# Optimization experiments

Measured on AMD Instinct MI355X. Metric: run time of the kernel, lower is better.

Reference implementation:

```python
import jax, jax.numpy as jnp
import numpy as np

N_NODES = 50000
N_EDGES = 800000
IN_DIM = 128
HIDDEN = 64
HEADS = 4
N_GRAPHS = 256
NEG_SLOPE = 0.2  # PyG GATConv default


def gat_conv(x, src, dst, W, a_src, a_dst, b):
    """PyG-style GATConv (concat=True), eval mode (no dropout).
    x: [N, F_in]; src/dst: [E] (self-loops already included);
    W: [H*C, F_in]; a_src/a_dst: [H, C]; b: [H*C].
    """
    N = x.shape[0]
    H, C = a_src.shape
    h = (x @ W.T).reshape(N, H, C)                      # [N, H, C]
    alo = (h * a_src[None]).sum(-1)                     # [N, H]
    ahi = (h * a_dst[None]).sum(-1)                     # [N, H]
    e = jax.nn.leaky_relu(alo[src] + ahi[dst], NEG_SLOPE)  # [E, H]
    # segment softmax over destination neighborhoods
    m = jax.ops.segment_max(e, dst, num_segments=N)     # [N, H]
    ex = jnp.exp(e - m[dst])
    denom = jax.ops.segment_sum(ex, dst, num_segments=N)
    alpha = ex / (denom[dst] + 1e-16)                   # [E, H]
    out = jax.ops.segment_sum(h[src] * alpha[:, :, None], dst, num_segments=N)
    return out.reshape(N, H * C) + b


def setup_inputs() -> dict:
    key = jax.random.key(0)
    ks = jax.random.split(key, 24)
    p = lambda k, s: (jax.random.normal(k, s, jnp.float32) * 0.1)
    x = jax.random.normal(ks[0], (N_NODES, IN_DIM), jnp.float32)
    edge_index = jax.random.randint(ks[1], (2, N_EDGES), 0, N_NODES, jnp.int64 if jax.config.jax_enable_x64 else jnp.int32)
    batch_idx = jnp.sort(jax.random.randint(ks[2], (N_NODES,), 0, N_GRAPHS))
    HC = HIDDEN * HEADS
    return {
        "x": x, "edge_index": edge_index, "batch_idx": batch_idx,
        "W1": p(ks[3], (HC, IN_DIM)), "as1": p(ks[4], (HEADS, HIDDEN)), "ad1": p(ks[5], (HEADS, HIDDEN)), "b1": jnp.zeros((HC,), jnp.float32),
        "W2": p(ks[6], (HC, HC)), "as2": p(ks[7], (HEADS, HIDDEN)), "ad2": p(ks[8], (HEADS, HIDDEN)), "b2": jnp.zeros((HC,), jnp.float32),
        "W3": p(ks[9], (HIDDEN, HC)), "as3": p(ks[10], (1, HIDDEN)), "ad3": p(ks[11], (1, HIDDEN)), "b3": jnp.zeros((HIDDEN,), jnp.float32),
        "Wc1": p(ks[12], (HIDDEN, HIDDEN)), "bc1": jnp.zeros((HIDDEN,), jnp.float32),
        "Wc2": p(ks[13], (1, HIDDEN)), "bc2": jnp.zeros((1,), jnp.float32),
        "Wr1": p(ks[14], (HIDDEN, HIDDEN)), "br1": jnp.zeros((HIDDEN,), jnp.float32),
        "Wr2": p(ks[15], (1, HIDDEN)), "br2": jnp.zeros((1,), jnp.float32),
    }


def reference(x, edge_index, batch_idx, W1, as1, ad1, b1, W2, as2, ad2, b2, W3, as3, ad3, b3, Wc1, bc1, Wc2, bc2, Wr1, br1, Wr2, br2):
    N = x.shape[0]
    loops = jnp.arange(N, dtype=edge_index.dtype)
    src = jnp.concatenate([edge_index[0], loops])  # add_self_loops=True (PyG default)
    dst = jnp.concatenate([edge_index[1], loops])
    h = jax.nn.elu(gat_conv(x, src, dst, W1, as1, ad1, b1))
    h = jax.nn.elu(gat_conv(h, src, dst, W2, as2, ad2, b2))
    h = jax.nn.elu(gat_conv(h, src, dst, W3, as3, ad3, b3))  # [N, HIDDEN]
    # global mean pool over graphs
    cnt = jax.ops.segment_sum(jnp.ones((N,), h.dtype), batch_idx, num_segments=N_GRAPHS)
    g = jax.ops.segment_sum(h, batch_idx, num_segments=N_GRAPHS) / jnp.maximum(cnt, 1.0)[:, None]
    cls_logit = (jax.nn.relu(g @ Wc1.T + bc1) @ Wc2.T + bc2).reshape(-1)
    reg_pred = (jax.nn.relu(g @ Wr1.T + br1) @ Wr2.T + br2).reshape(-1)
    return (cls_logit, reg_pred)
```

## Files before the change

### kernel.cpp

```cpp
#include <hip/hip_runtime.h>

#define N_NODES 50000
#define N_EDGES 800000
#define EP_EDGES (N_EDGES + N_NODES)
#define N_GRAPHS 256
#define NBLK_SCAN ((N_NODES + 255) / 256)
#define POOL_CHUNK ((N_NODES + 255) / 256)

typedef unsigned short u16;
typedef __attribute__((ext_vector_type(8))) short s8v;
typedef __attribute__((ext_vector_type(4))) float f4v;

__device__ __forceinline__ u16 fb(float f) {
  unsigned u = __float_as_uint(f);
  return (u16)((u + 0x7fffu + ((u >> 16) & 1u)) >> 16);
}
__device__ __forceinline__ float bfl(unsigned p) {
  return __uint_as_float(p << 16);
}
__device__ __forceinline__ float bfh(unsigned p) {
  return __uint_as_float(p & 0xffff0000u);
}
__device__ __forceinline__ float bff(u16 s) {
  return __uint_as_float(((unsigned)s) << 16);
}

#define F2B_N0 (N_NODES * 128)
#define F2B_N1 (F2B_N0 + 32768)
#define F2B_N2 (F2B_N1 + 65536)
#define F2B_N3 (F2B_N2 + 16384)
__global__ void f2b4(const float* __restrict__ x, const float* __restrict__ w1,
                     const float* __restrict__ w2, const float* __restrict__ w3,
                     u16* __restrict__ xb, u16* __restrict__ w1b,
                     u16* __restrict__ w2b, u16* __restrict__ w3b) {
  int i = blockIdx.x * 256 + threadIdx.x;
  if (i < F2B_N0) xb[i] = fb(x[i]);
  else if (i < F2B_N1) w1b[i - F2B_N0] = fb(w1[i - F2B_N0]);
  else if (i < F2B_N2) w2b[i - F2B_N1] = fb(w2[i - F2B_N1]);
  else if (i < F2B_N3) w3b[i - F2B_N2] = fb(w3[i - F2B_N2]);
}

__global__ __launch_bounds__(256) void gemm128(
    const u16* __restrict__ A, const u16* __restrict__ W,
    u16* __restrict__ C, int M, int Nout, int K) {
  __shared__ u16 As[128][40];
  __shared__ u16 Bs[128][40];
  const int t = threadIdx.x;
  const int m0 = blockIdx.y * 128, n0 = blockIdx.x * 128;
  const int rq = t >> 2, q = t & 3;
  const int w = t >> 6, lane = t & 63;
  const int wi = (w & 1) * 64, wj = (w >> 1) * 64;
  const int quad = lane >> 4, fr = lane & 15;

  f4v acc[4][4] = {};
  for (int k0 = 0; k0 < K; k0 += 32) {
    uint4 av[2], bv[2];
#pragma unroll
    for (int g = 0; g < 2; ++g) {
      int r = rq + g * 64;
      int m = m0 + r;
      av[g] = (m < M) ? *(const uint4*)&A[(size_t)m * K + k0 + q * 8]
                      : make_uint4(0, 0, 0, 0);
      bv[g] = *(const uint4*)&W[(size_t)(n0 + r) * K + k0 + q * 8];
    }
    __syncthreads();
#pragma unroll
    for (int g = 0; g < 2; ++g) {
      *(uint4*)&As[rq + g * 64][q * 8] = av[g];
      *(uint4*)&Bs[rq + g * 64][q * 8] = bv[g];
    }
    __syncthreads();
    s8v af[4], bf_[4];
#pragma unroll
    for (int i = 0; i < 4; ++i) {
      af[i] = *(const s8v*)&As[wi + i * 16 + fr][quad * 8];
      bf_[i] = *(const s8v*)&Bs[wj + i * 16 + fr][quad * 8];
    }
#pragma unroll
    for (int i = 0; i < 4; ++i)
#pragma unroll
      for (int j = 0; j < 4; ++j)
        acc[i][j] =
            __builtin_amdgcn_mfma_f32_16x16x32_bf16(af[i], bf_[j], acc[i][j], 0, 0, 0);
  }
#pragma unroll
  for (int i = 0; i < 4; ++i) {
    int rbase = m0 + wi + i * 16 + quad * 4;
#pragma unroll
    for (int j = 0; j < 4; ++j) {
      int col = n0 + wj + j * 16 + fr;
#pragma unroll
      for (int r = 0; r < 4; ++r) {
        int row = rbase + r;
        if (row < M) C[(size_t)row * Nout + col] = fb(acc[i][j][r]);
      }
    }
  }
}

__global__ __launch_bounds__(256) void gemm_bf16(
    const u16* __restrict__ A, const u16* __restrict__ W,
    u16* __restrict__ C, int M, int Nout, int K) {
  __shared__ u16 As[64][40];
  __shared__ u16 Bs[64][40];
  const int t = threadIdx.x;
  const int m0 = blockIdx.y * 64, n0 = blockIdx.x * 64;
  const int r = t >> 2, c = t & 3;
  const int w = t >> 6, lane = t & 63;
  const int mi = (w & 1) * 32, ni = (w >> 1) * 32;
  const int quad = lane >> 4, fr = lane & 15;

  f4v c00{}, c01{}, c10{}, c11{};
  for (int k0 = 0; k0 < K; k0 += 32) {
    uint4 av = make_uint4(0, 0, 0, 0);
    int m = m0 + r;
    if (m < M) av = *(const uint4*)&A[(size_t)m * K + k0 + c * 8];
    uint4 bv = *(const uint4*)&W[(size_t)(n0 + r) * K + k0 + c * 8];
    __syncthreads();
    *(uint4*)&As[r][c * 8] = av;
    *(uint4*)&Bs[r][c * 8] = bv;
    __syncthreads();
    s8v a0 = *(const s8v*)&As[mi + fr][quad * 8];
    s8v a1 = *(const s8v*)&As[mi + 16 + fr][quad * 8];
    s8v b0 = *(const s8v*)&Bs[ni + fr][quad * 8];
    s8v b1 = *(const s8v*)&Bs[ni + 16 + fr][quad * 8];
    c00 = __builtin_amdgcn_mfma_f32_16x16x32_bf16(a0, b0, c00, 0, 0, 0);
    c01 = __builtin_amdgcn_mfma_f32_16x16x32_bf16(a0, b1, c01, 0, 0, 0);
    c10 = __builtin_amdgcn_mfma_f32_16x16x32_bf16(a1, b0, c10, 0, 0, 0);
    c11 = __builtin_amdgcn_mfma_f32_16x16x32_bf16(a1, b1, c11, 0, 0, 0);
  }
  const int col = n0 + ni + fr;
#pragma unroll
  for (int i = 0; i < 4; ++i) {
    int row = m0 + mi + quad * 4 + i;
    if (row < M) {
      C[(size_t)row * Nout + col] = fb(c00[i]);
      C[(size_t)row * Nout + col + 16] = fb(c01[i]);
    }
    int row2 = row + 16;
    if (row2 < M) {
      C[(size_t)row2 * Nout + col] = fb(c10[i]);
      C[(size_t)row2 * Nout + col + 16] = fb(c11[i]);
    }
  }
}

__global__ void k_hist(const int* __restrict__ ei, int* __restrict__ deg) {
  int e = blockIdx.x * 256 + threadIdx.x;
  if (e >= EP_EDGES) return;
  int d = (e < N_EDGES) ? ei[N_EDGES + e] : e - N_EDGES;
  atomicAdd(&deg[d], 1);
}

__global__ void k_scan_local(const int* __restrict__ deg,
                             int* __restrict__ rowstart,
                             int* __restrict__ bsum) {
  __shared__ int sh[256];
  const int tid = threadIdx.x;
  const int i = blockIdx.x * 256 + tid;
  int v = (i < N_NODES) ? deg[i] : 0;
  sh[tid] = v;
  __syncthreads();
  for (int off = 1; off < 256; off <<= 1) {
    int add = (tid >= off) ? sh[tid - off] : 0;
    __syncthreads();
    sh[tid] += add;
    __syncthreads();
  }
  if (i < N_NODES) rowstart[i] = sh[tid] - v;
  if (tid == 255) bsum[blockIdx.x] = sh[255];
}

__global__ void k_scan_bsum(int* __restrict__ bsum, int* __restrict__ boff) {
  __shared__ int sh[256];
  const int tid = threadIdx.x;
  int v = (tid < NBLK_SCAN) ? bsum[tid] : 0;
  sh[tid] = v;
  __syncthreads();
  for (int off = 1; off < 256; off <<= 1) {
    int add = (tid >= off) ? sh[tid - off] : 0;
    __syncthreads();
    sh[tid] += add;
    __syncthreads();
  }
  boff[tid] = sh[tid] - v;
}

__global__ void k_scan_add(int* __restrict__ rowstart,
                           const int* __restrict__ boff) {
  int i = blockIdx.x * 256 + threadIdx.x;
  if (i < N_NODES) rowstart[i] += boff[i >> 8];
  if (i == N_NODES) rowstart[N_NODES] = EP_EDGES;
}

__global__ void k_scatter(const int* __restrict__ ei,
                          const int* __restrict__ rowstart,
                          int* __restrict__ fill, int* __restrict__ esrc) {
  int e = blockIdx.x * 256 + threadIdx.x;
  if (e >= EP_EDGES) return;
  int s, d;
  if (e < N_EDGES) { s = ei[e]; d = ei[N_EDGES + e]; }
  else             { s = d = e - N_EDGES; }
  int pos = rowstart[d] + atomicAdd(&fill[d], 1);
  esrc[pos] = s;
}

__global__ __launch_bounds__(256) void attn_scores4(
    const u16* __restrict__ h, const float* __restrict__ a_src,
    const float* __restrict__ a_dst, float* __restrict__ alo,
    float* __restrict__ ahi) {
  const int t = threadIdx.x;
  const int n = blockIdx.x * 4 + (t >> 6);
  const int lane = t & 63;
  const int head = lane >> 4, l16 = lane & 15;
  const int ch = head * 64 + l16 * 4;
  uint2 hv = *(const uint2*)&h[(size_t)n * 256 + ch];
  float4 asv = *(const float4*)&a_src[ch];
  float4 adv = *(const float4*)&a_dst[ch];
  float v0 = bfl(hv.x), v1 = bfh(hv.x), v2 = bfl(hv.y), v3 = bfh(hv.y);
  float s = v0 * asv.x + v1 * asv.y + v2 * asv.z + v3 * asv.w;
  float d = v0 * adv.x + v1 * adv.y + v2 * adv.z + v3 * adv.w;
#pragma unroll
  for (int off = 8; off; off >>= 1) {
    s += __shfl_xor(s, off, 64);
    d += __shfl_xor(d, off, 64);
  }
  if (l16 == 0) {
    alo[n * 4 + head] = s;
    ahi[n * 4 + head] = d;
  }
}

__global__ __launch_bounds__(256) void attn_scores1(
    const u16* __restrict__ h, const float* __restrict__ a_src,
    const float* __restrict__ a_dst, float* __restrict__ alo,
    float* __restrict__ ahi) {
  const int t = threadIdx.x;
  const int n = blockIdx.x * 4 + (t >> 6);
  const int lane = t & 63;
  float v = bff(h[(size_t)n * 64 + lane]);
  float s = v * a_src[lane];
  float d = v * a_dst[lane];
#pragma unroll
  for (int off = 32; off; off >>= 1) {
    s += __shfl_xor(s, off, 64);
    d += __shfl_xor(d, off, 64);
  }
  if (lane == 0) {
    alo[n] = s;
    ahi[n] = d;
  }
}

__global__ __launch_bounds__(64) void agg3_4(
    const int* __restrict__ rowstart, const int* __restrict__ esrc,
    const u16* __restrict__ hbuf, const float* __restrict__ alo,
    const float* __restrict__ ahi, const float* __restrict__ bias,
    u16* __restrict__ feat) {
  const int d = blockIdx.x;
  const int lane = threadIdx.x;
  const int head = lane >> 4;
  const int l16 = lane & 15;
  const int c = lane * 4;
  const int s0 = rowstart[d], s1 = rowstart[d + 1];
  const float ah = ahi[d * 4 + head];

  float sm = 0.f;
  for (int j = s0 + l16; j < s1; j += 16) {
    int s = esrc[j];
    float e = alo[s * 4 + head] + ah;
    e = e > 0.f ? e : 0.2f * e;
    sm += __expf(e);
  }
#pragma unroll
  for (int off = 8; off; off >>= 1) sm += __shfl_xor(sm, off, 64);
  const float linv = 1.f / (sm + 1e-16f);

  float o0 = 0.f, o1 = 0.f, o2 = 0.f, o3 = 0.f;
  for (int j = s0; j < s1; j += 4) {
    int ss[4];
    float wq[4];
#pragma unroll
    for (int q = 0; q < 4; ++q) {
      int jj = j + q;
      int sv = esrc[jj < EP_EDGES ? jj : EP_EDGES - 1];
      ss[q] = (jj < s1) ? sv : d;
    }
#pragma unroll
    for (int q = 0; q < 4; ++q) {
      float e = alo[ss[q] * 4 + head] + ah;
      e = e > 0.f ? e : 0.2f * e;
      wq[q] = (j + q < s1) ? __expf(e) * linv : 0.f;
    }
    uint2 hv[4];
#pragma unroll
    for (int q = 0; q < 4; ++q)
      hv[q] = *(const uint2*)&hbuf[(size_t)ss[q] * 256 + c];
#pragma unroll
    for (int q = 0; q < 4; ++q) {
      o0 += wq[q] * bfl(hv[q].x);
      o1 += wq[q] * bfh(hv[q].x);
      o2 += wq[q] * bfl(hv[q].y);
      o3 += wq[q] * bfh(hv[q].y);
    }
  }
  float4 bv = *(const float4*)&bias[c];
  float v0 = o0 + bv.x, v1 = o1 + bv.y, v2 = o2 + bv.z, v3 = o3 + bv.w;
  v0 = v0 > 0.f ? v0 : __expf(v0) - 1.f;
  v1 = v1 > 0.f ? v1 : __expf(v1) - 1.f;
  v2 = v2 > 0.f ? v2 : __expf(v2) - 1.f;
  v3 = v3 > 0.f ? v3 : __expf(v3) - 1.f;
  uint2 pv;
  pv.x = (unsigned)fb(v0) | ((unsigned)fb(v1) << 16);
  pv.y = (unsigned)fb(v2) | ((unsigned)fb(v3) << 16);
  *(uint2*)&feat[(size_t)d * 256 + c] = pv;
}

__global__ __launch_bounds__(64) void agg3_1(
    const int* __restrict__ rowstart, const int* __restrict__ esrc,
    const u16* __restrict__ hbuf, const float* __restrict__ alo,
    const float* __restrict__ ahi, const float* __restrict__ bias,
    float* __restrict__ feat) {
  const int d = blockIdx.x;
  const int t = threadIdx.x;
  const int s0 = rowstart[d], s1 = rowstart[d + 1];
  const float ah = ahi[d];

  float sm = 0.f;
  for (int j = s0 + t; j < s1; j += 64) {
    int s = esrc[j];
    float e = alo[s] + ah;
    e = e > 0.f ? e : 0.2f * e;
    sm += __expf(e);
  }
#pragma unroll
  for (int off = 32; off; off >>= 1) sm += __shfl_xor(sm, off, 64);
  const float linv = 1.f / (sm + 1e-16f);

  float o = 0.f;
  for (int j = s0; j < s1; j += 4) {
    int ss[4];
    float wq[4];
#pragma unroll
    for (int q = 0; q < 4; ++q) {
      int jj = j + q;
      int sv = esrc[jj < EP_EDGES ? jj : EP_EDGES - 1];
      ss[q] = (jj < s1) ? sv : d;
    }
#pragma unroll
    for (int q = 0; q < 4; ++q) {
      float e = alo[ss[q]] + ah;
      e = e > 0.f ? e : 0.2f * e;
      wq[q] = (j + q < s1) ? __expf(e) * linv : 0.f;
    }
    u16 hv[4];
#pragma unroll
    for (int q = 0; q < 4; ++q) hv[q] = hbuf[(size_t)ss[q] * 64 + t];
#pragma unroll
    for (int q = 0; q < 4; ++q) o += wq[q] * bff(hv[q]);
  }
  float v = o + bias[t];
  feat[(size_t)d * 64 + t] = v > 0.f ? v : __expf(v) - 1.f;
}

__global__ __launch_bounds__(64) void pool_seg(
    const float* __restrict__ feat, const int* __restrict__ batch,
    float* __restrict__ gsum, float* __restrict__ gcnt) {
  const int b = blockIdx.x;
  const int t = threadIdx.x;
  int n0 = b * POOL_CHUNK;
  int n1 = n0 + POOL_CHUNK;
  if (n1 > N_NODES) n1 = N_NODES;
  if (n0 >= n1) return;
  int g = batch[n0];
  float acc = 0.f;
  int cnt = 0;
  for (int n = n0; n < n1; ++n) {
    int gn = batch[n];
    if (gn != g) {
      atomicAdd(&gsum[g * 64 + t], acc);
      if (t == 0) atomicAdd(&gcnt[g], (float)cnt);
      acc = 0.f; cnt = 0; g = gn;
    }
    acc += feat[(size_t)n * 64 + t];
    ++cnt;
  }
  atomicAdd(&gsum[g * 64 + t], acc);
  if (t == 0) atomicAdd(&gcnt[g], (float)cnt);
}

__global__ void heads(const float* __restrict__ gsum,
                      const float* __restrict__ gcnt,
                      const float* __restrict__ Wc1, const float* __restrict__ bc1,
                      const float* __restrict__ Wc2, const float* __restrict__ bc2,
                      const float* __restrict__ Wr1, const float* __restrict__ br1,
                      const float* __restrict__ Wr2, const float* __restrict__ br2,
                      float* __restrict__ out) {
  __shared__ float g[64];
  const int gi = blockIdx.x, j = threadIdx.x;
  float cnt = gcnt[gi];
  cnt = cnt < 1.f ? 1.f : cnt;
  g[j] = gsum[gi * 64 + j] / cnt;
  __syncthreads();
  float hc = bc1[j], hr = br1[j];
#pragma unroll 8
  for (int c = 0; c < 64; ++c) {
    float gv = g[c];
    hc += gv * Wc1[j * 64 + c];
    hr += gv * Wr1[j * 64 + c];
  }
  hc = fmaxf(hc, 0.f) * Wc2[j];
  hr = fmaxf(hr, 0.f) * Wr2[j];
#pragma unroll
  for (int off = 32; off; off >>= 1) {
    hc += __shfl_down(hc, off, 64);
    hr += __shfl_down(hr, off, 64);
  }
  if (j == 0) {
    out[gi] = hc + bc2[0];
    out[N_GRAPHS + gi] = hr + br2[0];
  }
}

extern "C" void kernel_launch(void* const* d_in, const int* in_sizes, int n_in,
                              void* d_out, int out_size, void* d_ws,
                              size_t ws_size, hipStream_t stream) {
  const float* x   = (const float*)d_in[0];
  const int* ei    = (const int*)d_in[1];
  const int* batch = (const int*)d_in[2];
  const float* W1  = (const float*)d_in[3];
  const float* as1 = (const float*)d_in[4];
  const float* ad1 = (const float*)d_in[5];
  const float* b1  = (const float*)d_in[6];
  const float* W2  = (const float*)d_in[7];
  const float* as2 = (const float*)d_in[8];
  const float* ad2 = (const float*)d_in[9];
  const float* b2  = (const float*)d_in[10];
  const float* W3  = (const float*)d_in[11];
  const float* as3 = (const float*)d_in[12];
  const float* ad3 = (const float*)d_in[13];
  const float* b3  = (const float*)d_in[14];
  const float* Wc1 = (const float*)d_in[15];
  const float* bc1 = (const float*)d_in[16];
  const float* Wc2 = (const float*)d_in[17];
  const float* bc2 = (const float*)d_in[18];
  const float* Wr1 = (const float*)d_in[19];
  const float* br1 = (const float*)d_in[20];
  const float* Wr2 = (const float*)d_in[21];
  const float* br2 = (const float*)d_in[22];
  float* out = (float*)d_out;

  float* ws = (float*)d_ws;
  u16* h_buf = (u16*)ws;
  float* p = ws + (size_t)N_NODES * 128;
  u16* featb = (u16*)p;
  p += (size_t)N_NODES * 128;
  u16* xb = (u16*)p;
  p += (size_t)N_NODES * 64;
  u16* W1b = (u16*)p; p += 16384;
  u16* W2b = (u16*)p; p += 32768;
  u16* W3b = (u16*)p; p += 8192;
  float* feat3 = p;   p += (size_t)N_NODES * 64;
  float* alo   = p;   p += (size_t)N_NODES * 4;
  float* ahi   = p;   p += (size_t)N_NODES * 4;
  int* rowstart = (int*)p; p += (N_NODES + 4);
  int* esrc    = (int*)p;  p += EP_EDGES;
  float* gsum  = p;   p += N_GRAPHS * 64;
  float* gcnt  = p;
  int* deg  = (int*)alo;
  int* fill = (int*)alo + N_NODES;
  int* bsum = (int*)gsum;
  int* boff = (int*)gsum + 256;

  hipMemsetAsync(deg, 0, (size_t)2 * N_NODES * 4, stream);
  const int eblk = (EP_EDGES + 255) / 256;
  k_hist<<<eblk, 256, 0, stream>>>(ei, deg);
  k_scan_local<<<NBLK_SCAN, 256, 0, stream>>>(deg, rowstart, bsum);
  k_scan_bsum<<<1, 256, 0, stream>>>(bsum, boff);
  k_scan_add<<<(N_NODES + 256) / 256, 256, 0, stream>>>(rowstart, boff);
  k_scatter<<<eblk, 256, 0, stream>>>(ei, rowstart, fill, esrc);

  f2b4<<<(F2B_N3 + 255) / 256, 256, 0, stream>>>(x, W1, W2, W3, xb, W1b, W2b,
                                                 W3b);

  const int MB128 = (N_NODES + 127) / 128;
  const int MB64 = (N_NODES + 63) / 64;
  gemm128<<<dim3(2, MB128), 256, 0, stream>>>(xb, W1b, h_buf, N_NODES, 256, 128);
  attn_scores4<<<N_NODES / 4, 256, 0, stream>>>(h_buf, as1, ad1, alo, ahi);
  agg3_4<<<N_NODES, 64, 0, stream>>>(rowstart, esrc, h_buf, alo, ahi, b1,
                                     featb);
  gemm128<<<dim3(2, MB128), 256, 0, stream>>>(featb, W2b, h_buf, N_NODES, 256, 256);
  attn_scores4<<<N_NODES / 4, 256, 0, stream>>>(h_buf, as2, ad2, alo, ahi);
  agg3_4<<<N_NODES, 64, 0, stream>>>(rowstart, esrc, h_buf, alo, ahi, b2,
                                     featb);
  gemm_bf16<<<dim3(1, MB64), 256, 0, stream>>>(featb, W3b, h_buf, N_NODES, 64, 256);
  attn_scores1<<<N_NODES / 4, 256, 0, stream>>>(h_buf, as3, ad3, alo, ahi);
  agg3_1<<<N_NODES, 64, 0, stream>>>(rowstart, esrc, h_buf, alo, ahi, b3,
                                     feat3);

  hipMemsetAsync(gsum, 0, (size_t)(N_GRAPHS * 64 + N_GRAPHS) * 4, stream);
  pool_seg<<<N_GRAPHS, 64, 0, stream>>>(feat3, batch, gsum, gcnt);
  heads<<<N_GRAPHS, 64, 0, stream>>>(gsum, gcnt, Wc1, bc1, Wc2, bc2, Wr1, br1,
                                     Wr2, br2, out);
}
```

Baseline: 562.7 us.

## Fuse attention score computation into GEMM epilogue and fold x conversion into GEMM

Computes per-head source/destination attention scores directly from the fp32 GEMM accumulators in the epilogue, removing the separate attn_scores4 kernels and their re-read of h. The first layer GEMM now reads fp32 x and converts to bf16 while loading, which removes the standalone x conversion pass and its bf16 buffer. The aggregation loops are also unrolled to 8 neighbours per iteration so more gathers are in flight. Scores now come from unrounded fp32 accumulators rather than bf16-rounded h, and the wider unroll raises register pressure.

```diff
diff --git a/kernel.cpp b/kernel.cpp
--- a/kernel.cpp
+++ b/kernel.cpp
@@ -25,24 +25,60 @@
   return __uint_as_float(((unsigned)s) << 16);
 }
 
-#define F2B_N0 (N_NODES * 128)
-#define F2B_N1 (F2B_N0 + 32768)
-#define F2B_N2 (F2B_N1 + 65536)
-#define F2B_N3 (F2B_N2 + 16384)
-__global__ void f2b4(const float* __restrict__ x, const float* __restrict__ w1,
-                     const float* __restrict__ w2, const float* __restrict__ w3,
-                     u16* __restrict__ xb, u16* __restrict__ w1b,
+#define W_N1 32768
+#define W_N2 (W_N1 + 65536)
+#define W_N3 (W_N2 + 16384)
+__global__ void f2bw(const float* __restrict__ w1, const float* __restrict__ w2,
+                     const float* __restrict__ w3, u16* __restrict__ w1b,
                      u16* __restrict__ w2b, u16* __restrict__ w3b) {
   int i = blockIdx.x * 256 + threadIdx.x;
-  if (i < F2B_N0) xb[i] = fb(x[i]);
-  else if (i < F2B_N1) w1b[i - F2B_N0] = fb(w1[i - F2B_N0]);
-  else if (i < F2B_N2) w2b[i - F2B_N1] = fb(w2[i - F2B_N1]);
-  else if (i < F2B_N3) w3b[i - F2B_N2] = fb(w3[i - F2B_N2]);
+  if (i < W_N1) w1b[i] = fb(w1[i]);
+  else if (i < W_N2) w2b[i - W_N1] = fb(w2[i - W_N1]);
+  else if (i < W_N3) w3b[i - W_N2] = fb(w3[i - W_N2]);
+}
+
+__device__ __forceinline__ void score_epilogue(
+    f4v (&acc)[4][4], const float* __restrict__ a_src,
+    const float* __restrict__ a_dst, float* __restrict__ alo,
+    float* __restrict__ ahi, int m0, int n0, int wi, int wj, int quad, int fr,
+    int M) {
+  const int head = (n0 + wj) >> 6;
+  float as[4], ad[4];
+#pragma unroll
+  for (int j = 0; j < 4; ++j) {
+    int col = n0 + wj + j * 16 + fr;
+    as[j] = a_src[col];
+    ad[j] = a_dst[col];
+  }
+#pragma unroll
+  for (int i = 0; i < 4; ++i) {
+#pragma unroll
+    for (int r = 0; r < 4; ++r) {
+      float s = 0.f, d = 0.f;
+#pragma unroll
+      for (int j = 0; j < 4; ++j) {
+        s += acc[i][j][r] * as[j];
+        d += acc[i][j][r] * ad[j];
+      }
+#pragma unroll
+      for (int off = 8; off; off >>= 1) {
+        s += __shfl_xor(s, off, 64);
+        d += __shfl_xor(d, off, 64);
+      }
+      int row = m0 + wi + i * 16 + quad * 4 + r;
+      if (fr == 0 && row < M) {
+        alo[row * 4 + head] = s;
+        ahi[row * 4 + head] = d;
+      }
+    }
+  }
 }
 
 __global__ __launch_bounds__(256) void gemm128(
     const u16* __restrict__ A, const u16* __restrict__ W,
-    u16* __restrict__ C, int M, int Nout, int K) {
+    u16* __restrict__ C, const float* __restrict__ a_src,
+    const float* __restrict__ a_dst, float* __restrict__ alo,
+    float* __restrict__ ahi, int M, int Nout, int K) {
   __shared__ u16 As[128][40];
   __shared__ u16 Bs[128][40];
   const int t = threadIdx.x;
@@ -96,6 +132,76 @@
       }
     }
   }
+  score_epilogue(acc, a_src, a_dst, alo, ahi, m0, n0, wi, wj, quad, fr, M);
+}
+
+__global__ __launch_bounds__(256) void gemm128_f32(
+    const float* __restrict__ A, const u16* __restrict__ W,
+    u16* __restrict__ C, const float* __restrict__ a_src,
+    const float* __restrict__ a_dst, float* __restrict__ alo,
+    float* __restrict__ ahi, int M, int Nout, int K) {
+  __shared__ u16 As[128][40];
+  __shared__ u16 Bs[128][40];
+  const int t = threadIdx.x;
+  const int m0 = blockIdx.y * 128, n0 = blockIdx.x * 128;
+  const int rq = t >> 2, q = t & 3;
+  const int w = t >> 6, lane = t & 63;
+  const int wi = (w & 1) * 64, wj = (w >> 1) * 64;
+  const int quad = lane >> 4, fr = lane & 15;
+
+  f4v acc[4][4] = {};
+  for (int k0 = 0; k0 < K; k0 += 32) {
+    uint4 av[2], bv[2];
+#pragma unroll
+    for (int g = 0; g < 2; ++g) {
+      int r = rq + g * 64;
+      int m = m0 + r;
+      if (m < M) {
+        float4 f0 = *(const float4*)&A[(size_t)m * K + k0 + q * 8];
+        float4 f1 = *(const float4*)&A[(size_t)m * K + k0 + q * 8 + 4];
+        av[g].x = (unsigned)fb(f0.x) | ((unsigned)fb(f0.y) << 16);
+        av[g].y = (unsigned)fb(f0.z) | ((unsigned)fb(f0.w) << 16);
+        av[g].z = (unsigned)fb(f1.x) | ((unsigned)fb(f1.y) << 16);
+        av[g].w = (unsigned)fb(f1.z) | ((unsigned)fb(f1.w) << 16);
+      } else {
+        av[g] = make_uint4(0, 0, 0, 0);
+      }
+      bv[g] = *(const uint4*)&W[(size_t)(n0 + r) * K + k0 + q * 8];
+    }
+    __syncthreads();
+#pragma unroll
+    for (int g = 0; g < 2; ++g) {
+      *(uint4*)&As[rq + g * 64][q * 8] = av[g];
+      *(uint4*)&Bs[rq + g * 64][q * 8] = bv[g];
+    }
+    __syncthreads();
+    s8v af[4], bf_[4];
+#pragma unroll
+    for (int i = 0; i < 4; ++i) {
+      af[i] = *(const s8v*)&As[wi + i * 16 + fr][quad * 8];
+      bf_[i] = *(const s8v*)&Bs[wj + i * 16 + fr][quad * 8];
+    }
+#pragma unroll
+    for (int i = 0; i < 4; ++i)
+#pragma unroll
+      for (int j = 0; j < 4; ++j)
+        acc[i][j] =
+            __builtin_amdgcn_mfma_f32_16x16x32_bf16(af[i], bf_[j], acc[i][j], 0, 0, 0);
+  }
+#pragma unroll
+  for (int i = 0; i < 4; ++i) {
+    int rbase = m0 + wi + i * 16 + quad * 4;
+#pragma unroll
+    for (int j = 0; j < 4; ++j) {
+      int col = n0 + wj + j * 16 + fr;
+#pragma unroll
+      for (int r = 0; r < 4; ++r) {
+        int row = rbase + r;
+        if (row < M) C[(size_t)row * Nout + col] = fb(acc[i][j][r]);
+      }
+    }
+  }
+  score_epilogue(acc, a_src, a_dst, alo, ahi, m0, n0, wi, wj, quad, fr, M);
 }
 
 __global__ __launch_bounds__(256) void gemm_bf16(
@@ -203,32 +309,6 @@
   else             { s = d = e - N_EDGES; }
   int pos = rowstart[d] + atomicAdd(&fill[d], 1);
   esrc[pos] = s;
-}
-
-__global__ __launch_bounds__(256) void attn_scores4(
-    const u16* __restrict__ h, const float* __restrict__ a_src,
-    const float* __restrict__ a_dst, float* __restrict__ alo,
-    float* __restrict__ ahi) {
-  const int t = threadIdx.x;
-  const int n = blockIdx.x * 4 + (t >> 6);
-  const int lane = t & 63;
-  const int head = lane >> 4, l16 = lane & 15;
-  const int ch = head * 64 + l16 * 4;
-  uint2 hv = *(const uint2*)&h[(size_t)n * 256 + ch];
-  float4 asv = *(const float4*)&a_src[ch];
-  float4 adv = *(const float4*)&a_dst[ch];
-  float v0 = bfl(hv.x), v1 = bfh(hv.x), v2 = bfl(hv.y), v3 = bfh(hv.y);
-  float s = v0 * asv.x + v1 * asv.y + v2 * asv.z + v3 * asv.w;
-  float d = v0 * adv.x + v1 * adv.y + v2 * adv.z + v3 * adv.w;
-#pragma unroll
-  for (int off = 8; off; off >>= 1) {
-    s += __shfl_xor(s, off, 64);
-    d += __shfl_xor(d, off, 64);
-  }
-  if (l16 == 0) {
-    alo[n * 4 + head] = s;
-    ahi[n * 4 + head] = d;
-  }
 }
 
 __global__ __launch_bounds__(256) void attn_scores1(
@@ -277,27 +357,27 @@
   const float linv = 1.f / (sm + 1e-16f);
 
   float o0 = 0.f, o1 = 0.f, o2 = 0.f, o3 = 0.f;
-  for (int j = s0; j < s1; j += 4) {
-    int ss[4];
-    float wq[4];
-#pragma unroll
-    for (int q = 0; q < 4; ++q) {
+  for (int j = s0; j < s1; j += 8) {
+    int ss[8];
+    float wq[8];
+#pragma unroll
+    for (int q = 0; q < 8; ++q) {
       int jj = j + q;
       int sv = esrc[jj < EP_EDGES ? jj : EP_EDGES - 1];
       ss[q] = (jj < s1) ? sv : d;
     }
 #pragma unroll
-    for (int q = 0; q < 4; ++q) {
+    for (int q = 0; q < 8; ++q) {
       float e = alo[ss[q] * 4 + head] + ah;
       e = e > 0.f ? e : 0.2f * e;
       wq[q] = (j + q < s1) ? __expf(e) * linv : 0.f;
     }
-    uint2 hv[4];
-#pragma unroll
-    for (int q = 0; q < 4; ++q)
+    uint2 hv[8];
+#pragma unroll
+    for (int q = 0; q < 8; ++q)
       hv[q] = *(const uint2*)&hbuf[(size_t)ss[q] * 256 + c];
 #pragma unroll
-    for (int q = 0; q < 4; ++q) {
+    for (int q = 0; q < 8; ++q) {
       o0 += wq[q] * bfl(hv[q].x);
       o1 += wq[q] * bfh(hv[q].x);
       o2 += wq[q] * bfl(hv[q].y);
@@ -338,26 +418,26 @@
   const float linv = 1.f / (sm + 1e-16f);
 
   float o = 0.f;
-  for (int j = s0; j < s1; j += 4) {
-    int ss[4];
-    float wq[4];
-#pragma unroll
-    for (int q = 0; q < 4; ++q) {
+  for (int j = s0; j < s1; j += 8) {
+    int ss[8];
+    float wq[8];
+#pragma unroll
+    for (int q = 0; q < 8; ++q) {
       int jj = j + q;
       int sv = esrc[jj < EP_EDGES ? jj : EP_EDGES - 1];
       ss[q] = (jj < s1) ? sv : d;
     }
 #pragma unroll
-    for (int q = 0; q < 4; ++q) {
+    for (int q = 0; q < 8; ++q) {
       float e = alo[ss[q]] + ah;
       e = e > 0.f ? e : 0.2f * e;
       wq[q] = (j + q < s1) ? __expf(e) * linv : 0.f;
     }
-    u16 hv[4];
-#pragma unroll
-    for (int q = 0; q < 4; ++q) hv[q] = hbuf[(size_t)ss[q] * 64 + t];
-#pragma unroll
-    for (int q = 0; q < 4; ++q) o += wq[q] * bff(hv[q]);
+    u16 hv[8];
+#pragma unroll
+    for (int q = 0; q < 8; ++q) hv[q] = hbuf[(size_t)ss[q] * 64 + t];
+#pragma unroll
+    for (int q = 0; q < 8; ++q) o += wq[q] * bff(hv[q]);
   }
   float v = o + bias[t];
   feat[(size_t)d * 64 + t] = v > 0.f ? v : __expf(v) - 1.f;
@@ -455,8 +535,6 @@
   float* p = ws + (size_t)N_NODES * 128;
   u16* featb = (u16*)p;
   p += (size_t)N_NODES * 128;
-  u16* xb = (u16*)p;
-  p += (size_t)N_NODES * 64;
   u16* W1b = (u16*)p; p += 16384;
   u16* W2b = (u16*)p; p += 32768;
   u16* W3b = (u16*)p; p += 8192;
@@ -480,17 +558,16 @@
   k_scan_add<<<(N_NODES + 256) / 256, 256, 0, stream>>>(rowstart, boff);
   k_scatter<<<eblk, 256, 0, stream>>>(ei, rowstart, fill, esrc);
 
-  f2b4<<<(F2B_N3 + 255) / 256, 256, 0, stream>>>(x, W1, W2, W3, xb, W1b, W2b,
-                                                 W3b);
+  f2bw<<<(W_N3 + 255) / 256, 256, 0, stream>>>(W1, W2, W3, W1b, W2b, W3b);
 
   const int MB128 = (N_NODES + 127) / 128;
   const int MB64 = (N_NODES + 63) / 64;
-  gemm128<<<dim3(2, MB128), 256, 0, stream>>>(xb, W1b, h_buf, N_NODES, 256, 128);
-  attn_scores4<<<N_NODES / 4, 256, 0, stream>>>(h_buf, as1, ad1, alo, ahi);
+  gemm128_f32<<<dim3(2, MB128), 256, 0, stream>>>(x, W1b, h_buf, as1, ad1, alo,
+                                                  ahi, N_NODES, 256, 128);
   agg3_4<<<N_NODES, 64, 0, stream>>>(rowstart, esrc, h_buf, alo, ahi, b1,
                                      featb);
-  gemm128<<<dim3(2, MB128), 256, 0, stream>>>(featb, W2b, h_buf, N_NODES, 256, 256);
-  attn_scores4<<<N_NODES / 4, 256, 0, stream>>>(h_buf, as2, ad2, alo, ahi);
+  gemm128<<<dim3(2, MB128), 256, 0, stream>>>(featb, W2b, h_buf, as2, ad2, alo,
+                                              ahi, N_NODES, 256, 256);
   agg3_4<<<N_NODES, 64, 0, stream>>>(rowstart, esrc, h_buf, alo, ahi, b2,
                                      featb);
   gemm_bf16<<<dim3(1, MB64), 256, 0, stream>>>(featb, W3b, h_buf, N_NODES, 64, 256);
```

New measurement: 558.7 us. About the same (-0.7%).
